# Optimization experiments

Measured on AMD Instinct MI355X. Metric: run time of the kernel, lower is better.

The kernel has to match this reference:

```python
import jax, jax.numpy as jnp
import numpy as np

N_NODES = 50000


def gcn_conv(x, W, b, src, dst, norm, n):
    # x: [N, Fin]; W: [Fin, Fout]; src/dst/norm: [E+N] (self-loops included)
    h = x @ W                                   # dense transform first (PyG order)
    msg = h[src] * norm[:, None]                # gather + per-edge scale
    out = jax.ops.segment_sum(msg, dst, num_segments=n)  # scatter-add aggregate
    return out + b


def setup_inputs() -> dict:
    key = jax.random.key(0)
    k1, k2, k3, k4 = jax.random.split(key, 4)
    F_IN, H, C, E = 64, 64, 16, 800000
    x = jax.random.normal(k1, (N_NODES, F_IN), dtype=jnp.float32)
    edge_index = jax.random.randint(k2, (2, E), 0, N_NODES, dtype=jnp.int64)
    W1 = jax.random.normal(k3, (F_IN, H), dtype=jnp.float32) * (1.0 / np.sqrt(F_IN))
    b1 = jnp.zeros((H,), dtype=jnp.float32)
    W2 = jax.random.normal(k4, (H, C), dtype=jnp.float32) * (1.0 / np.sqrt(H))
    b2 = jnp.zeros((C,), dtype=jnp.float32)
    return {"x": x, "edge_index": edge_index, "W1": W1, "b1": b1, "W2": W2, "b2": b2}


def reference(x, edge_index, W1, b1, W2, b2):
    n = x.shape[0]
    loops = jnp.arange(n, dtype=edge_index.dtype)
    src = jnp.concatenate([edge_index[0], loops])  # GCN adds self-loops
    dst = jnp.concatenate([edge_index[1], loops])
    # symmetric normalization: deg^{-1/2}[src] * deg^{-1/2}[dst], deg over dst
    deg = jax.ops.segment_sum(jnp.ones_like(dst, dtype=x.dtype), dst, num_segments=n)
    dinv = jax.lax.rsqrt(deg)  # deg >= 1 due to self-loops
    norm = dinv[src] * dinv[dst]
    h = gcn_conv(x, W1, b1, src, dst, norm, n)
    h = jax.nn.relu(h)
    out = gcn_conv(h, W2, b2, src, dst, norm, n)
    return out
```

## Files before the change

kernel.cpp:

```cpp
#include <hip/hip_runtime.h>

#define N_NODES 50000
#define N_EDGES 800000
#define F1 64
#define F2 16
#define NBINS 196
#define BIN_SHIFT 8
#define EPB 8192
#define NSB ((N_EDGES + EPB - 1) / EPB)
#define TBW 200
#define STAGE_MAX 6144
#define G1_ROWS 32
#define G1_NB ((N_NODES + G1_ROWS - 1) / G1_ROWS)

typedef _Float16 half_t;
typedef __attribute__((ext_vector_type(8))) _Float16 half8;
typedef __attribute__((ext_vector_type(4))) _Float16 half4;

__global__ void __launch_bounds__(256) k_bs_gemm1(
        const int* __restrict__ src, const int* __restrict__ dst,
        unsigned* __restrict__ pairs, int* __restrict__ table,
        const float* __restrict__ x, const float* __restrict__ W1,
        half_t* __restrict__ h0h) {
    __shared__ int smem[1024 + EPB];
    int t = threadIdx.x;

    if (blockIdx.x < NSB) {
        int* hist    = smem;
        int* loff    = smem + 256;
        int* lcur    = smem + 512;
        int* scanbuf = smem + 768;
        unsigned* stage = (unsigned*)(smem + 1024);
        int blk = blockIdx.x;
        int e0 = blk * EPB;
        int eend = min(e0 + EPB, N_EDGES);
        int n = eend - e0;

        for (int i = t; i < NBINS; i += 256) hist[i] = 0;
        __syncthreads();
        for (int e = e0 + t; e < eend; e += 256)
            atomicAdd(&hist[dst[e] >> BIN_SHIFT], 1);
        __syncthreads();
        int v = (t < NBINS) ? hist[t] : 0;
        scanbuf[t] = v;
        __syncthreads();
        for (int s = 1; s < 256; s <<= 1) {
            int u = (t >= s) ? scanbuf[t - s] : 0;
            __syncthreads();
            scanbuf[t] += u;
            __syncthreads();
        }
        if (t < NBINS) { loff[t] = scanbuf[t] - v; lcur[t] = scanbuf[t] - v; }
        if (t == 0) loff[NBINS] = n;
        __syncthreads();
        for (int e = e0 + t; e < eend; e += 256) {
            int d = dst[e];
            int b = d >> BIN_SHIFT;
            int pos = atomicAdd(&lcur[b], 1);
            stage[pos] = (unsigned)src[e] | ((unsigned)(d & 255) << 16);
        }
        if (t <= NBINS) table[blk * TBW + t] = loff[t];
        __syncthreads();
        for (int i = t; i < n; i += 256) pairs[e0 + i] = stage[i];
    } else {
        float* Ws = (float*)smem;
        int bid = blockIdx.x - NSB;
        int lane = t & 63, wid = t >> 6;
        for (int i = t; i < F1 * F1; i += 256) Ws[i] = W1[i];
        int row0 = bid * G1_ROWS + wid * 8;
        float xv[8], acc[8];
#pragma unroll
        for (int r = 0; r < 8; ++r) {
            int row = row0 + r;
            xv[r] = (row < N_NODES) ? x[row * F1 + lane] : 0.f;
            acc[r] = 0.f;
        }
        __syncthreads();
#pragma unroll
        for (int k = 0; k < F1; ++k) {
            float w = Ws[k * F1 + lane];
#pragma unroll
            for (int r = 0; r < 8; ++r) {
                float xs = __int_as_float(
                    __builtin_amdgcn_readlane(__float_as_int(xv[r]), k));
                acc[r] = fmaf(xs, w, acc[r]);
            }
        }
#pragma unroll
        for (int r = 0; r < 8; ++r) {
            int row = row0 + r;
            if (row < N_NODES) h0h[row * F1 + lane] = (half_t)acc[r];
        }
    }
}

__global__ void __launch_bounds__(1024) k_binsort(
        const int* __restrict__ table, const unsigned* __restrict__ pairs,
        float* __restrict__ dinv, int* __restrict__ node_start,
        unsigned short* __restrict__ csr) {
    __shared__ int segoff[NSB], segcnt[NSB], segdst[NSB];
    __shared__ int scanbuf[256], colsum[256], hist[256], lcur[256];
    __shared__ unsigned stage[STAGE_MAX];
    __shared__ unsigned short sorted[STAGE_MAX];
    int t = threadIdx.x, b = blockIdx.x;

    if (t < 256) hist[t] = 0;

    int c = 0, cs = 0;
    if (t < NSB) {
        int o = table[t * TBW + b];
        segoff[t] = o;
        cs = o;
        c = table[t * TBW + b + 1] - o;
        segcnt[t] = c;
    }
    if (t < 256) { scanbuf[t] = c; colsum[t] = cs; }
    __syncthreads();
    for (int s = 1; s < 256; s <<= 1) {
        int u = 0, u2 = 0;
        if (t < 256 && t >= s) { u = scanbuf[t - s]; u2 = colsum[t - s]; }
        __syncthreads();
        if (t < 256) { scanbuf[t] += u; colsum[t] += u2; }
        __syncthreads();
    }
    if (t < NSB) segdst[t] = scanbuf[t] - c;
    int n = scanbuf[255];
    int bstart = colsum[255];
    __syncthreads();

    int grp = t >> 4, gl = t & 15;
    for (int k = grp; k < NSB; k += 64) {
        int sc = segcnt[k], base = k * EPB + segoff[k], sd = segdst[k];
        for (int i = gl; i < sc; i += 16) stage[sd + i] = pairs[base + i];
    }
    __syncthreads();

    for (int i = t; i < n; i += 1024) atomicAdd(&hist[stage[i] >> 16], 1);
    __syncthreads();

    int lo = b << BIN_SHIFT;
    int nb = min(256, N_NODES - lo);
    int dg = (t < 256) ? hist[t] : 0;
    if (t < 256) scanbuf[t] = dg;
    __syncthreads();
    for (int s = 1; s < 256; s <<= 1) {
        int u = 0;
        if (t < 256 && t >= s) u = scanbuf[t - s];
        __syncthreads();
        if (t < 256) scanbuf[t] += u;
        __syncthreads();
    }
    if (t < 256) {
        int pr = scanbuf[t] - dg;
        lcur[t] = pr;
        if (t < nb) {
            dinv[lo + t] = rsqrtf(1.0f + (float)dg);
            node_start[lo + t] = bstart + pr;
        }
    }
    if (b == NBINS - 1 && t == 0) node_start[N_NODES] = N_EDGES;
    __syncthreads();

    for (int i = t; i < n; i += 1024) {
        unsigned p = stage[i];
        int pos = atomicAdd(&lcur[p >> 16], 1);
        sorted[pos] = (unsigned short)(p & 0xFFFF);
    }
    __syncthreads();
    for (int i = t; i < n; i += 1024) csr[bstart + i] = sorted[i];
}

__global__ void __launch_bounds__(256) k_gather1f(
        const int* __restrict__ node_start, const unsigned short* __restrict__ csr,
        const float* __restrict__ dinv, const half8* __restrict__ h08,
        const float* __restrict__ b1, const float* __restrict__ W2,
        half_t* __restrict__ h1h) {
    int t = threadIdx.x;
    int lane = t & 63, wid = t >> 6;
    int j = lane >> 3, f = lane & 7;
    int g = lane >> 4, c = lane & 15;

    int d = blockIdx.x * 4 + wid;
    int start = node_start[d], end = node_start[d + 1];

    float w2r[16];
#pragma unroll
    for (int kk = 0; kk < 16; ++kk) w2r[kk] = W2[(g * 16 + kk) * 16 + c];
    const float4* b14 = (const float4*)b1;
    float4 bA = b14[f * 2], bB = b14[f * 2 + 1];

    float acc[8] = {0.f, 0.f, 0.f, 0.f, 0.f, 0.f, 0.f, 0.f};
    int i = start + j;
    for (; i + 8 < end; i += 16) {
        int s0 = csr[i], s1 = csr[i + 8];
        float w0 = dinv[s0], w1 = dinv[s1];
        half8 v0 = h08[s0 * 8 + f], v1 = h08[s1 * 8 + f];
#pragma unroll
        for (int q = 0; q < 8; ++q)
            acc[q] += w0 * (float)v0[q] + w1 * (float)v1[q];
    }
    if (i < end) {
        int s = csr[i];
        float w = dinv[s];
        half8 v = h08[s * 8 + f];
#pragma unroll
        for (int q = 0; q < 8; ++q) acc[q] += w * (float)v[q];
    }
#pragma unroll
    for (int m = 8; m <= 32; m <<= 1)
#pragma unroll
        for (int q = 0; q < 8; ++q) acc[q] += __shfl_xor(acc[q], m);

    float dd = dinv[d];
    half8 sv = h08[d * 8 + f];
    float r[8];
    {
        const float* ba = (const float*)&bA;
        const float* bb = (const float*)&bB;
#pragma unroll
        for (int q = 0; q < 8; ++q) {
            float bq = (q < 4) ? ba[q] : bb[q - 4];
            r[q] = fmaxf(dd * (acc[q] + dd * (float)sv[q]) + bq, 0.f);
        }
    }

    float p = 0.f;
#pragma unroll
    for (int kk = 0; kk < 16; ++kk) {
        int srcf = 2 * g + (kk >> 3);
        p += __shfl(r[kk & 7], srcf) * w2r[kk];
    }
    p += __shfl_xor(p, 16);
    p += __shfl_xor(p, 32);
    if (g == 0) h1h[d * F2 + c] = (half_t)(dd * p);
}

__global__ void __launch_bounds__(256) k_gather2(
        const int* __restrict__ node_start, const unsigned short* __restrict__ csr,
        const float* __restrict__ dinv, const half4* __restrict__ h14,
        const float4* __restrict__ b24, float4* __restrict__ out4) {
    int t = threadIdx.x;
    int lane = t & 63;
    int j = lane >> 2, f = lane & 3;
    int d = blockIdx.x * 4 + (t >> 6);
    int start = node_start[d], end = node_start[d + 1];
    float acc[4] = {0.f, 0.f, 0.f, 0.f};
    int i = start + j;
    for (; i + 16 < end; i += 32) {
        int s0 = csr[i], s1 = csr[i + 16];
        half4 v0 = h14[s0 * 4 + f], v1 = h14[s1 * 4 + f];
#pragma unroll
        for (int q = 0; q < 4; ++q) acc[q] += (float)v0[q] + (float)v1[q];
    }
    if (i < end) {
        int s = csr[i];
        half4 v = h14[s * 4 + f];
#pragma unroll
        for (int q = 0; q < 4; ++q) acc[q] += (float)v[q];
    }
#pragma unroll
    for (int m = 4; m <= 32; m <<= 1)
#pragma unroll
        for (int q = 0; q < 4; ++q) acc[q] += __shfl_xor(acc[q], m);

    if (j == 0) {
        float dd = dinv[d];
        half4 sv = h14[d * 4 + f];
        float4 bb = b24[f];
        float4 r;
        r.x = bb.x + dd * (acc[0] + (float)sv[0]);
        r.y = bb.y + dd * (acc[1] + (float)sv[1]);
        r.z = bb.z + dd * (acc[2] + (float)sv[2]);
        r.w = bb.w + dd * (acc[3] + (float)sv[3]);
        out4[d * 4 + f] = r;
    }
}

extern "C" void kernel_launch(void* const* d_in, const int* in_sizes, int n_in,
                              void* d_out, int out_size, void* d_ws, size_t ws_size,
                              hipStream_t stream) {
    const float* x  = (const float*)d_in[0];
    const int*   ei = (const int*)d_in[1];
    const float* W1 = (const float*)d_in[2];
    const float* b1 = (const float*)d_in[3];
    const float* W2 = (const float*)d_in[4];
    const float* b2 = (const float*)d_in[5];
    float* out = (float*)d_out;

    const int* src = ei;
    const int* dst = ei + N_EDGES;

    int*            table      = (int*)d_ws;
    float*          dinv       = (float*)d_ws + 40960;
    int*            node_start = (int*)d_ws + 91008;
    unsigned short* csr        = (unsigned short*)((int*)d_ws + 141056);
    unsigned*       pairs      = (unsigned*)d_ws + 541056;
    half_t*         h0h        = (half_t*)((int*)d_ws + 1345056);
    half_t*         h1h        = (half_t*)((int*)d_ws + 2945056);

    k_bs_gemm1<<<NSB + G1_NB, 256, 0, stream>>>(src, dst, pairs, table, x, W1, h0h);
    k_binsort <<<NBINS, 1024, 0, stream>>>(table, pairs, dinv, node_start, csr);
    k_gather1f<<<N_NODES / 4, 256, 0, stream>>>(node_start, csr, dinv, (const half8*)h0h,
                                                b1, W2, h1h);
    k_gather2 <<<N_NODES / 4, 256, 0, stream>>>(node_start, csr, dinv, (const half4*)h1h,
                                                (const float4*)b2, (float4*)out);
}
```

Before: 150.2 us.

## Split dense transform across both bin-sort kernels and vectorize bin pass

```diff
diff --git a/kernel.cpp b/kernel.cpp
--- a/kernel.cpp
+++ b/kernel.cpp
@@ -6,168 +6,201 @@
 #define F2 16
 #define NBINS 196
 #define BIN_SHIFT 8
-#define EPB 8192
+#define EPB 4096
 #define NSB ((N_EDGES + EPB - 1) / EPB)
 #define TBW 200
 #define STAGE_MAX 6144
-#define G1_ROWS 32
+#define G1_ROWS 128
 #define G1_NB ((N_NODES + G1_ROWS - 1) / G1_ROWS)
+#define G1_A  196
 
 typedef _Float16 half_t;
 typedef __attribute__((ext_vector_type(8))) _Float16 half8;
 typedef __attribute__((ext_vector_type(4))) _Float16 half4;
 
-__global__ void __launch_bounds__(256) k_bs_gemm1(
+__device__ __forceinline__ void gemm1_body(int bid, const float* __restrict__ x,
+                                           const float* __restrict__ W1,
+                                           half_t* __restrict__ h0h,
+                                           float* __restrict__ Ws) {
+    int t = threadIdx.x;
+    int lane = t & 63, wid = t >> 6;
+    for (int i = t; i < F1 * F1; i += 1024) Ws[i] = W1[i];
+    int row0 = bid * G1_ROWS + wid * 8;
+    float xv[8], acc[8];
+#pragma unroll
+    for (int r = 0; r < 8; ++r) {
+        int row = row0 + r;
+        xv[r] = (row < N_NODES) ? x[row * F1 + lane] : 0.f;
+        acc[r] = 0.f;
+    }
+    __syncthreads();
+#pragma unroll
+    for (int k = 0; k < F1; ++k) {
+        float w = Ws[k * F1 + lane];
+#pragma unroll
+        for (int r = 0; r < 8; ++r) {
+            float xs = __int_as_float(
+                __builtin_amdgcn_readlane(__float_as_int(xv[r]), k));
+            acc[r] = fmaf(xs, w, acc[r]);
+        }
+    }
+#pragma unroll
+    for (int r = 0; r < 8; ++r) {
+        int row = row0 + r;
+        if (row < N_NODES) h0h[row * F1 + lane] = (half_t)acc[r];
+    }
+}
+
+__global__ void __launch_bounds__(1024) k_bsA(
         const int* __restrict__ src, const int* __restrict__ dst,
         unsigned* __restrict__ pairs, int* __restrict__ table,
         const float* __restrict__ x, const float* __restrict__ W1,
         half_t* __restrict__ h0h) {
-    __shared__ int smem[1024 + EPB];
+    __shared__ int smem[1056 + EPB];
     int t = threadIdx.x;
 
     if (blockIdx.x < NSB) {
         int* hist    = smem;
         int* loff    = smem + 256;
-        int* lcur    = smem + 512;
-        int* scanbuf = smem + 768;
-        unsigned* stage = (unsigned*)(smem + 1024);
+        int* lcur    = smem + 514;
+        int* scanbuf = smem + 770;
+        unsigned* stage = (unsigned*)(smem + 1056);
         int blk = blockIdx.x;
         int e0 = blk * EPB;
         int eend = min(e0 + EPB, N_EDGES);
         int n = eend - e0;
 
-        for (int i = t; i < NBINS; i += 256) hist[i] = 0;
-        __syncthreads();
-        for (int e = e0 + t; e < eend; e += 256)
-            atomicAdd(&hist[dst[e] >> BIN_SHIFT], 1);
-        __syncthreads();
-        int v = (t < NBINS) ? hist[t] : 0;
-        scanbuf[t] = v;
+        if (t < 256) hist[t] = 0;
+        __syncthreads();
+        for (int e = e0 + 4 * t; e < eend; e += 4096) {
+            int4 d4 = *(const int4*)(dst + e);
+            atomicAdd(&hist[d4.x >> BIN_SHIFT], 1);
+            atomicAdd(&hist[d4.y >> BIN_SHIFT], 1);
+            atomicAdd(&hist[d4.z >> BIN_SHIFT], 1);
+            atomicAdd(&hist[d4.w >> BIN_SHIFT], 1);
+        }
+        __syncthreads();
+        if (t < 256) scanbuf[t] = hist[t];
         __syncthreads();
         for (int s = 1; s < 256; s <<= 1) {
-            int u = (t >= s) ? scanbuf[t - s] : 0;
-            __syncthreads();
-            scanbuf[t] += u;
-            __syncthreads();
-        }
-        if (t < NBINS) { loff[t] = scanbuf[t] - v; lcur[t] = scanbuf[t] - v; }
+            int u = 0;
+            if (t < 256 && t >= s) u = scanbuf[t - s];
+            __syncthreads();
+            if (t < 256) scanbuf[t] += u;
+            __syncthreads();
+        }
+        if (t < 256) { int v = hist[t]; loff[t] = scanbuf[t] - v; lcur[t] = scanbuf[t] - v; }
         if (t == 0) loff[NBINS] = n;
         __syncthreads();
-        for (int e = e0 + t; e < eend; e += 256) {
-            int d = dst[e];
-            int b = d >> BIN_SHIFT;
-            int pos = atomicAdd(&lcur[b], 1);
-            stage[pos] = (unsigned)src[e] | ((unsigned)(d & 255) << 16);
+        for (int e = e0 + 4 * t; e < eend; e += 4096) {
+            int4 d4 = *(const int4*)(dst + e);
+            int4 s4 = *(const int4*)(src + e);
+            int p;
+            p = atomicAdd(&lcur[d4.x >> BIN_SHIFT], 1);
+            stage[p] = (unsigned)s4.x | ((unsigned)(d4.x & 255) << 16);
+            p = atomicAdd(&lcur[d4.y >> BIN_SHIFT], 1);
+            stage[p] = (unsigned)s4.y | ((unsigned)(d4.y & 255) << 16);
+            p = atomicAdd(&lcur[d4.z >> BIN_SHIFT], 1);
+            stage[p] = (unsigned)s4.z | ((unsigned)(d4.z & 255) << 16);
+            p = atomicAdd(&lcur[d4.w >> BIN_SHIFT], 1);
+            stage[p] = (unsigned)s4.w | ((unsigned)(d4.w & 255) << 16);
         }
         if (t <= NBINS) table[blk * TBW + t] = loff[t];
         __syncthreads();
-        for (int i = t; i < n; i += 256) pairs[e0 + i] = stage[i];
+        for (int i = 4 * t; i < n; i += 4096)
+            *(uint4*)(pairs + e0 + i) = *(const uint4*)(stage + i);
     } else {
-        float* Ws = (float*)smem;
-        int bid = blockIdx.x - NSB;
-        int lane = t & 63, wid = t >> 6;
-        for (int i = t; i < F1 * F1; i += 256) Ws[i] = W1[i];
-        int row0 = bid * G1_ROWS + wid * 8;
-        float xv[8], acc[8];
-#pragma unroll
-        for (int r = 0; r < 8; ++r) {
-            int row = row0 + r;
-            xv[r] = (row < N_NODES) ? x[row * F1 + lane] : 0.f;
-            acc[r] = 0.f;
-        }
-        __syncthreads();
-#pragma unroll
-        for (int k = 0; k < F1; ++k) {
-            float w = Ws[k * F1 + lane];
-#pragma unroll
-            for (int r = 0; r < 8; ++r) {
-                float xs = __int_as_float(
-                    __builtin_amdgcn_readlane(__float_as_int(xv[r]), k));
-                acc[r] = fmaf(xs, w, acc[r]);
-            }
-        }
-#pragma unroll
-        for (int r = 0; r < 8; ++r) {
-            int row = row0 + r;
-            if (row < N_NODES) h0h[row * F1 + lane] = (half_t)acc[r];
-        }
-    }
-}
-
-__global__ void __launch_bounds__(1024) k_binsort(
+        gemm1_body(blockIdx.x - NSB, x, W1, h0h, (float*)smem);
+    }
+}
+
+__global__ void __launch_bounds__(1024) k_bsB(
         const int* __restrict__ table, const unsigned* __restrict__ pairs,
         float* __restrict__ dinv, int* __restrict__ node_start,
-        unsigned short* __restrict__ csr) {
-    __shared__ int segoff[NSB], segcnt[NSB], segdst[NSB];
-    __shared__ int scanbuf[256], colsum[256], hist[256], lcur[256];
-    __shared__ unsigned stage[STAGE_MAX];
-    __shared__ unsigned short sorted[STAGE_MAX];
-    int t = threadIdx.x, b = blockIdx.x;
-
-    if (t < 256) hist[t] = 0;
-
-    int c = 0, cs = 0;
-    if (t < NSB) {
-        int o = table[t * TBW + b];
-        segoff[t] = o;
-        cs = o;
-        c = table[t * TBW + b + 1] - o;
-        segcnt[t] = c;
-    }
-    if (t < 256) { scanbuf[t] = c; colsum[t] = cs; }
-    __syncthreads();
-    for (int s = 1; s < 256; s <<= 1) {
-        int u = 0, u2 = 0;
-        if (t < 256 && t >= s) { u = scanbuf[t - s]; u2 = colsum[t - s]; }
-        __syncthreads();
-        if (t < 256) { scanbuf[t] += u; colsum[t] += u2; }
-        __syncthreads();
-    }
-    if (t < NSB) segdst[t] = scanbuf[t] - c;
-    int n = scanbuf[255];
-    int bstart = colsum[255];
-    __syncthreads();
-
-    int grp = t >> 4, gl = t & 15;
-    for (int k = grp; k < NSB; k += 64) {
-        int sc = segcnt[k], base = k * EPB + segoff[k], sd = segdst[k];
-        for (int i = gl; i < sc; i += 16) stage[sd + i] = pairs[base + i];
-    }
-    __syncthreads();
-
-    for (int i = t; i < n; i += 1024) atomicAdd(&hist[stage[i] >> 16], 1);
-    __syncthreads();
-
-    int lo = b << BIN_SHIFT;
-    int nb = min(256, N_NODES - lo);
-    int dg = (t < 256) ? hist[t] : 0;
-    if (t < 256) scanbuf[t] = dg;
-    __syncthreads();
-    for (int s = 1; s < 256; s <<= 1) {
-        int u = 0;
-        if (t < 256 && t >= s) u = scanbuf[t - s];
-        __syncthreads();
-        if (t < 256) scanbuf[t] += u;
-        __syncthreads();
-    }
-    if (t < 256) {
-        int pr = scanbuf[t] - dg;
-        lcur[t] = pr;
-        if (t < nb) {
-            dinv[lo + t] = rsqrtf(1.0f + (float)dg);
-            node_start[lo + t] = bstart + pr;
-        }
-    }
-    if (b == NBINS - 1 && t == 0) node_start[N_NODES] = N_EDGES;
-    __syncthreads();
-
-    for (int i = t; i < n; i += 1024) {
-        unsigned p = stage[i];
-        int pos = atomicAdd(&lcur[p >> 16], 1);
-        sorted[pos] = (unsigned short)(p & 0xFFFF);
-    }
-    __syncthreads();
-    for (int i = t; i < n; i += 1024) csr[bstart + i] = sorted[i];
+        unsigned short* __restrict__ csr, const float* __restrict__ x,
+        const float* __restrict__ W1, half_t* __restrict__ h0h) {
+    __shared__ int smem[10832];
+    int t = threadIdx.x;
+
+    if (blockIdx.x < NBINS) {
+        int* segoff  = smem;
+        int* segcnt  = smem + 196;
+        int* segdst  = smem + 392;
+        int* scanbuf = smem + 588;
+        int* colsum  = smem + 844;
+        int* hist    = smem + 1100;
+        int* lcur    = smem + 1356;
+        unsigned* stage = (unsigned*)(smem + 1612);
+        unsigned short* sorted = (unsigned short*)(smem + 7756);
+        int b = blockIdx.x;
+
+        if (t < 256) hist[t] = 0;
+
+        int c = 0, cs = 0;
+        if (t < NSB) {
+            int o = table[t * TBW + b];
+            segoff[t] = o;
+            cs = o;
+            c = table[t * TBW + b + 1] - o;
+            segcnt[t] = c;
+        }
+        if (t < 256) { scanbuf[t] = c; colsum[t] = cs; }
+        __syncthreads();
+        for (int s = 1; s < 256; s <<= 1) {
+            int u = 0, u2 = 0;
+            if (t < 256 && t >= s) { u = scanbuf[t - s]; u2 = colsum[t - s]; }
+            __syncthreads();
+            if (t < 256) { scanbuf[t] += u; colsum[t] += u2; }
+            __syncthreads();
+        }
+        if (t < NSB) segdst[t] = scanbuf[t] - c;
+        int n = scanbuf[255];
+        int bstart = colsum[255];
+        __syncthreads();
+
+        int grp = t >> 4, gl = t & 15;
+        for (int k = grp; k < NSB; k += 64) {
+            int sc = segcnt[k], base = k * EPB + segoff[k], sd = segdst[k];
+            for (int i = gl; i < sc; i += 16) stage[sd + i] = pairs[base + i];
+        }
+        __syncthreads();
+
+        for (int i = t; i < n; i += 1024) atomicAdd(&hist[stage[i] >> 16], 1);
+        __syncthreads();
+
+        int lo = b << BIN_SHIFT;
+        int nb = min(256, N_NODES - lo);
+        int dg = (t < 256) ? hist[t] : 0;
+        if (t < 256) scanbuf[t] = dg;
+        __syncthreads();
+        for (int s = 1; s < 256; s <<= 1) {
+            int u = 0;
+            if (t < 256 && t >= s) u = scanbuf[t - s];
+            __syncthreads();
+            if (t < 256) scanbuf[t] += u;
+            __syncthreads();
+        }
+        if (t < 256) {
+            int pr = scanbuf[t] - dg;
+            lcur[t] = pr;
+            if (t < nb) {
+                dinv[lo + t] = rsqrtf(1.0f + (float)dg);
+                node_start[lo + t] = bstart + pr;
+            }
+        }
+        if (b == NBINS - 1 && t == 0) node_start[N_NODES] = N_EDGES;
+        __syncthreads();
+
+        for (int i = t; i < n; i += 1024) {
+            unsigned p = stage[i];
+            int pos = atomicAdd(&lcur[p >> 16], 1);
+            sorted[pos] = (unsigned short)(p & 0xFFFF);
+        }
+        __syncthreads();
+        for (int i = t; i < n; i += 1024) csr[bstart + i] = sorted[i];
+    } else {
+        gemm1_body(blockIdx.x, x, W1, h0h, (float*)smem);
+    }
 }
 
 __global__ void __launch_bounds__(256) k_gather1f(
@@ -298,8 +331,9 @@
     half_t*         h0h        = (half_t*)((int*)d_ws + 1345056);
     half_t*         h1h        = (half_t*)((int*)d_ws + 2945056);
 
-    k_bs_gemm1<<<NSB + G1_NB, 256, 0, stream>>>(src, dst, pairs, table, x, W1, h0h);
-    k_binsort <<<NBINS, 1024, 0, stream>>>(table, pairs, dinv, node_start, csr);
+    k_bsA<<<NSB + G1_A, 1024, 0, stream>>>(src, dst, pairs, table, x, W1, h0h);
+    k_bsB<<<NBINS + (G1_NB - G1_A), 1024, 0, stream>>>(table, pairs, dinv, node_start,
+                                                       csr, x, W1, h0h);
     k_gather1f<<<N_NODES / 4, 256, 0, stream>>>(node_start, csr, dinv, (const half8*)h0h,
                                                 b1, W2, h1h);
     k_gather2 <<<N_NODES / 4, 256, 0, stream>>>(node_start, csr, dinv, (const half4*)h1h,
```

After: 156.3 us. 4.1% more time.
